# Kernel tuning notes

Hardware: AMD Instinct MI355X
Metric: run time of the kernel (lower is better)

The kernel has to match this reference:

```python
import jax, jax.numpy as jnp
import numpy as np

N_DIST, H, W, K = 256, 256, 192, 129
DR, DR0, DELTA = 0.2, 0.2, 1e-11


def _dual_exp(d, b1, b2, b3, b4):
    return b1 * np.exp(-b2 * d) + b3 * np.exp(-b4 * d)


def setup_inputs() -> dict:
    key = jax.random.key(0)
    d = (np.arange(N_DIST) + 1.0) * DR                      # distances (cm)
    gaus_amp = _dual_exp(d, 1.0, 0.01, 0.1, 0.001)
    gaus_sig = 0.05 * d + 1.0
    bkg_amp = _dual_exp(d, 0.05, 0.05, 0.01, 0.005)
    bkg_sig = 0.08 * d + 2.0
    xk = np.arange(-(K // 2), K // 2 + 1) * DR / DR0        # (K,) kernel coords
    # gaussian kernel (get_gaus_layer)
    kernel_g = np.sqrt(gaus_amp)[:, None] * np.exp(-xk[None, :] ** 2 / (2 * gaus_sig[:, None] ** 2 + DELTA))
    # background kernels (get_bkg_layers) with emulated splines
    w_f = lambda t: np.exp(-np.abs(t))
    iso_f = lambda t: 1.0 / (1.0 + t ** 2)
    xw = xk[None, :] / bkg_sig[:, None]
    kernel_w = bkg_amp[:, None] * (DR / DR0) * w_f(xw)
    kernel_iso = bkg_amp[:, None] * (DR / DR0) * iso_f(xw)
    # normalization factor (configure)
    xs = np.linspace(-5.0, 5.0, 2001)
    Iw = np.trapz(w_f(xs), xs)
    Iiso = np.trapz(iso_f(xs), xs)
    Nw = 3 * bkg_amp * Iw * bkg_sig
    Niso = bkg_amp * Iiso * bkg_sig
    Ng2 = gaus_amp * 2 * np.pi * gaus_sig ** 2 * (DR0 / DR) ** 2
    norm = (Nw + Niso ** 2 + 1.0) * Ng2
    x = jax.random.uniform(key, (1, N_DIST, H, W), dtype=jnp.float32)
    return {
        "x": x,
        "kernel_g": jnp.asarray(kernel_g, jnp.float32),
        "kernel_w": jnp.asarray(kernel_w, jnp.float32),
        "kernel_iso": jnp.asarray(kernel_iso, jnp.float32),
        "norm": jnp.asarray(norm, jnp.float32),
    }


def _dwconv(x, kern, axis):
    """Depthwise 'same' Conv1d along `axis` of (N,H,W); channels = dim 0."""
    n = x.shape[0]
    perm = (2, 0, 1) if axis == 1 else (1, 0, 2)   # -> (batch, channels=N, length)
    inv = (1, 2, 0) if axis == 1 else (1, 0, 2)
    xb = jnp.transpose(x, perm)
    y = jax.lax.conv_general_dilated(
        xb, kern[:, None, :], (1,), 'SAME',
        feature_group_count=n, dimension_numbers=('NCH', 'OIH', 'NCH'))
    return jnp.transpose(y, inv)


def _rotate(x, ang):
    """Bilinear rotation of (N,S,S) in dims (1,2), zero padding (grid_sample-like)."""
    s = x.shape[1]
    c = (s - 1) * 0.5
    ca, sa = jnp.cos(ang), jnp.sin(ang)
    idx = jnp.arange(s, dtype=x.dtype) - c
    yy, xx = jnp.meshgrid(idx, idx, indexing='ij')
    sy = ca * yy + sa * xx + c   # inverse-rotated source coords
    sx = -sa * yy + ca * xx + c
    y0 = jnp.floor(sy)
    x0 = jnp.floor(sx)
    fy, fx = sy - y0, sx - x0
    y0i, x0i = y0.astype(jnp.int32), x0.astype(jnp.int32)

    def gat(yi, xi):
        valid = (yi >= 0) & (yi < s) & (xi >= 0) & (xi < s)
        v = x[:, jnp.clip(yi, 0, s - 1), jnp.clip(xi, 0, s - 1)]
        return jnp.where(valid, v, 0.0)

    return (gat(y0i, x0i) * (1 - fy) * (1 - fx)
            + gat(y0i, x0i + 1) * (1 - fy) * fx
            + gat(y0i + 1, x0i) * fy * (1 - fx)
            + gat(y0i + 1, x0i + 1) * fy * fx)


def reference(x, kernel_g, kernel_w, kernel_iso, norm):
    out = x[0]                                   # (N, H, W)
    out = _dwconv(out, kernel_g, 1)
    out = _dwconv(out, kernel_g, 2)
    iso = _dwconv(out, kernel_iso, 1)
    iso = _dwconv(iso, kernel_iso, 2)
    n, h, w = out.shape
    pad = (n - w) // 2
    padded = jnp.pad(out, ((0, 0), (0, 0), (pad, pad)))  # (N, H, H) square plane
    tails = jnp.zeros_like(padded)
    for i in range(3):                            # 0, 60, 120 degrees
        ang = float(np.deg2rad(60 * i))
        t = _rotate(padded, ang)
        t = _dwconv(t, kernel_w, 2)
        tails = tails + _rotate(t, -ang)
    tails = tails[:, :, pad:pad + w]
    out = (out + tails + iso) / norm[:, None, None]
    return out[None]
```

## Files before the change

kernel.cpp:

```cpp
#include <hip/hip_runtime.h>
#include <cmath>

#define CN   256
#define HN   256
#define WN   192
#define KN   129
#define RN   64
#define SN   256
#define PADN 32

#define BBR 92
#define BBP 96


template <int TW, int WD, bool ACC>
__global__ __launch_bounds__(512, 2) void conv_w_blk(const float* __restrict__ in,
                                                     const float* __restrict__ kern,
                                                     float* __restrict__ out) {
    constexpr int NO    = TW / 8;
    constexpr int TOTB  = (NO + 128) / 8;
    constexpr int PITCH = 196;
    static_assert(NO == 16, "this instantiation is tuned for NO=16");
    __shared__ float lds[64 * PITCH + 132];
    float* __restrict__ ldsK = lds + 64 * PITCH;
    const int tid = threadIdx.x;
    const int x0  = blockIdx.x * TW;
    const int h0  = blockIdx.y * 64;
    const int c   = blockIdx.z;
    const float* __restrict__ in_c = in + ((size_t)c * HN + h0) * WD;

    if (tid < 132) ldsK[tid] = (tid < KN) ? kern[c * KN + tid] : 0.f;

    const int gc0 = max(0, x0 - 64);
    {
        const int srow = tid >> 3;
        const int scg  = tid & 7;
#pragma unroll
        for (int m = 0; m < 6; ++m) {
            const int c4 = scg + 8 * m;
            *(float4*)(lds + srow * PITCH + 4 * c4) =
                *(const float4*)(in_c + (size_t)srow * WD + gc0 + 4 * c4);
        }
    }
    __syncthreads();

    const int wv  = tid >> 6;
    const int l   = tid & 63;
    const int ac0 = x0 + wv * NO - 64;
    const int lbase = l * PITCH + (ac0 - gc0);

    float acc[NO];
#pragma unroll
    for (int t = 0; t < NO; ++t) acc[t] = 0.f;

    float X[8][8];

#define RD8(G)                                                                \
    if ((G) < TOTB) {                                                         \
        const int ac_ = ac0 + 8 * (G);                                        \
        if (ac_ >= 0 && ac_ + 8 <= WD) {             \
            const float4 a_ = *(const float4*)(lds + lbase + 8 * (G));        \
            const float4 b_ = *(const float4*)(lds + lbase + 8 * (G) + 4);    \
            X[(G) & 7][0] = a_.x; X[(G) & 7][1] = a_.y;                       \
            X[(G) & 7][2] = a_.z; X[(G) & 7][3] = a_.w;                       \
            X[(G) & 7][4] = b_.x; X[(G) & 7][5] = b_.y;                       \
            X[(G) & 7][6] = b_.z; X[(G) & 7][7] = b_.w;                       \
        } else {                                                              \
            _Pragma("unroll")                                                 \
            for (int i_ = 0; i_ < 8; ++i_) {                                  \
                const int cc_ = ac_ + i_;                                     \
                const int cl_ = min(max(cc_, 0), WD - 1);                     \
                const float v_ = lds[l * PITCH + (cl_ - gc0)];                \
                X[(G) & 7][i_] = (cc_ == cl_) ? v_ : 0.f;                     \
            }                                                                 \
        }                                                                     \
    }

    RD8(0) RD8(1) RD8(2) RD8(3) RD8(4) RD8(5)

    const float4* __restrict__ k4 = (const float4*)ldsK;
#pragma unroll
    for (int s = 0; s < 4; ++s) {
        float4 kc = k4[8 * s];
#pragma unroll
        for (int q = 0; q < 8; ++q) {
            float4 kn = (q < 7) ? k4[8 * s + q + 1] : kc;
#pragma unroll
            for (int u = 0; u < 4; ++u) {
                const float kj = (u == 0) ? kc.x : (u == 1) ? kc.y
                               : (u == 2) ? kc.z : kc.w;
#pragma unroll
                for (int t = 0; t < NO; ++t) {
                    const int e = 4 * q + u + t;
                    acc[t] = fmaf(X[(4 * s + e / 8) & 7][e % 8], kj, acc[t]);
                }
            }
            if (q == 0) { RD8(4 * s + 6) }
            if (q == 1) { RD8(4 * s + 7) }
            if (q == 2) { RD8(4 * s + 8) }
            if (q == 4) { RD8(4 * s + 9) }
            kc = kn;
        }
    }
    {
        const float k128 = ldsK[128];
#pragma unroll
        for (int t = 0; t < NO; ++t) {
            const int e = 32 + t;
            acc[t] = fmaf(X[(12 + e / 8) & 7][e % 8], k128, acc[t]);
        }
    }
#undef RD8

    __syncthreads();
#pragma unroll
    for (int i = 0; i < NO; i += 4)
        *(float4*)(lds + l * PITCH + wv * NO + i) =
            make_float4(acc[i], acc[i + 1], acc[i + 2], acc[i + 3]);
    __syncthreads();
    float* __restrict__ obase = out + ((size_t)c * HN + h0) * WD + x0;
    constexpr int NF4 = (64 * TW / 4) / 512;
#pragma unroll
    for (int k = 0; k < NF4; ++k) {
        const int i4  = k * 512 + tid;
        const int r   = i4 / (TW / 4);
        const int c4o = i4 - r * (TW / 4);
        float4 v = *(const float4*)(lds + r * PITCH + 4 * c4o);
        if (ACC) {
            const float4 o = *(const float4*)(obase + (size_t)r * WD + 4 * c4o);
            v.x += o.x; v.y += o.y; v.z += o.z; v.w += o.w;
        }
        *(float4*)(obase + (size_t)r * WD + 4 * c4o) = v;
    }
}

template <int TW, int WD, bool ACC>
__global__ __launch_bounds__(512, 2) void conv_w_lds(const float* __restrict__ in,
                                                     const float* __restrict__ kern,
                                                     float* __restrict__ out) {
    constexpr int NO    = TW / 8;
    constexpr int TWW   = TW + 128;
    constexpr int PITCH = TWW + 1;
    constexpr int NB    = (2 * NO + 31) / NO;
    __shared__ float lds[64 * PITCH + 132];
    float* __restrict__ ldsK = lds + 64 * PITCH;
    const int tid = threadIdx.x;
    const int x0  = blockIdx.x * TW;
    const int h0  = blockIdx.y * 64;
    const int c   = blockIdx.z;
    const float* __restrict__ in_c = in + ((size_t)c * HN + h0) * WD;

    if (tid < 132) ldsK[tid] = (tid < KN) ? kern[c * KN + tid] : 0.f;

    const int colg = tid & 63;
    const int rr   = tid >> 6;
    const int off  = x0 - 64;

    if (off >= 0 && off + TWW <= WD) {
#pragma unroll
        for (int m = 0; m < 4; ++m) {
            if (colg + 64 * m < TWW) {
#pragma unroll
                for (int k = 0; k < 8; ++k)
                    lds[(rr + 8 * k) * PITCH + colg + 64 * m] =
                        in_c[(size_t)(rr + 8 * k) * WD + off + colg + 64 * m];
            }
        }
    } else {
#pragma unroll
        for (int m = 0; m < 4; ++m) {
            if (colg + 64 * m < TWW) {
#pragma unroll
                for (int k = 0; k < 8; ++k) {
                    int g  = off + colg + 64 * m;
                    int gc = min(max(g, 0), WD - 1);
                    float v = in_c[(size_t)(rr + 8 * k) * WD + gc];
                    lds[(rr + 8 * k) * PITCH + colg + 64 * m] = (g == gc) ? v : 0.f;
                }
            }
        }
    }
    __syncthreads();

    const int wv = tid >> 6;
    const int l  = tid & 63;
    const int base = l * PITCH + wv * NO;

    float acc[NO];
#pragma unroll
    for (int t = 0; t < NO; ++t) acc[t] = 0.f;

    float H[4][NO];
    const float4* __restrict__ k4 = (const float4*)ldsK;
#pragma unroll
    for (int s = 0; s < 4; ++s) {
        const int sb = base + 32 * s;
#pragma unroll
        for (int k = 0; k < NB - 1; ++k)
#pragma unroll
            for (int i = 0; i < NO; ++i) H[k][i] = lds[sb + k * NO + i];
        float4 kc = k4[8 * s];
#pragma unroll
        for (int q = 0; q < 8; ++q) {
            float4 kn = (q < 7) ? k4[8 * s + q + 1] : kc;
#pragma unroll
            for (int u = 0; u < 4; ++u) {
                const int up = 4 * q + u;
                const float kj = (u == 0) ? kc.x : (u == 1) ? kc.y
                               : (u == 2) ? kc.z : kc.w;
#pragma unroll
                for (int t = 0; t < NO; ++t) {
                    const int e = up + t;
                    const float val = (e < NO)     ? H[0][e]
                                    : (e < 2 * NO) ? H[1][e - NO]
                                    : (e < 3 * NO) ? H[2][e - 2 * NO]
                                                   : H[3][e - 3 * NO];
                    acc[t] = fmaf(val, kj, acc[t]);
                }
            }
            if (q == 0) {
#pragma unroll
                for (int i = 0; i < NO; ++i)
                    H[NB - 1][i] = lds[sb + (NB - 1) * NO + i];
            }
            kc = kn;
        }
        if (s == 3) {
            const float k128 = ldsK[128];
#pragma unroll
            for (int t = 0; t < NO; ++t) {
                const int e = 32 + t;
                const float val = (e < NO)     ? H[0][e]
                                : (e < 2 * NO) ? H[1][e - NO]
                                : (e < 3 * NO) ? H[2][e - 2 * NO]
                                               : H[3][e - 3 * NO];
                acc[t] = fmaf(val, k128, acc[t]);
            }
        }
    }

    __syncthreads();
#pragma unroll
    for (int i = 0; i < NO; ++i) lds[base + i] = acc[i];
    __syncthreads();
    float* __restrict__ obase = out + ((size_t)c * HN + h0) * WD + x0;
#pragma unroll
    for (int k = 0; k < (64 * TW) / 512; ++k) {
        const int idx = k * 512 + tid;
        const int r  = idx / TW;
        const int cl = idx - r * TW;
        float v = lds[r * PITCH + cl];
        if (ACC) v += obase[(size_t)r * WD + cl];
        obase[(size_t)r * WD + cl] = v;
    }
}

__global__ __launch_bounds__(512, 2) void conv_h_lds(const float* __restrict__ in,
                                                     const float* __restrict__ kern,
                                                     float* __restrict__ out) {
    __shared__ float lds[256 * 64 + 132];
    float* __restrict__ ldsK = lds + 256 * 64;
    const int tid = threadIdx.x;
    const int x0  = blockIdx.x * 64;
    const int h0  = blockIdx.y * 128;
    const int c   = blockIdx.z;
    const float* __restrict__ in_c = in + (size_t)c * HN * WN + x0;

    if (tid < 132) ldsK[tid] = (tid < KN) ? kern[c * KN + tid] : 0.f;

    {
        const int f4 = (tid & 15) * 4;
        const int rw = tid >> 4;
        const int off = h0 - 64;
#pragma unroll
        for (int p = 0; p < 8; ++p) {
            const int lr = rw + 32 * p;
            const int g  = off + lr;
            const int gc = min(max(g, 0), HN - 1);
            float4 v = *(const float4*)(in_c + (size_t)gc * WN + f4);
            if (g != gc) { v.x = 0.f; v.y = 0.f; v.z = 0.f; v.w = 0.f; }
            *(float4*)(lds + lr * 64 + f4) = v;
        }
    }
    __syncthreads();

    const int W = (tid >> 6) * 16;
    const int l = tid & 63;

    float acc[16];
#pragma unroll
    for (int t = 0; t < 16; ++t) acc[t] = 0.f;

    float X0[16], X1[16], X2[16], X3[16];

#define RD16(BUF, b)                                                          \
    { _Pragma("unroll")                                                       \
      for (int i = 0; i < 16; ++i) BUF[i] = lds[(W + 16 * (b) + i) * 64 + l]; }

#define STG(s, LOW, MID, HIGH, NXT, hasNxt)                                   \
    {                                                                         \
        const float4* __restrict__ k4 = (const float4*)ldsK;                  \
        float4 kc = k4[8 * (s)];                                              \
        _Pragma("unroll")                                                     \
        for (int q = 0; q < 8; ++q) {                                         \
            float4 kn = (q < 7) ? k4[8 * (s) + q + 1] : kc;                   \
            _Pragma("unroll")                                                 \
            for (int u = 0; u < 4; ++u) {                                     \
                const float kj = (u == 0) ? kc.x : (u == 1) ? kc.y            \
                               : (u == 2) ? kc.z : kc.w;                      \
                _Pragma("unroll")                                             \
                for (int t = 0; t < 16; ++t) {                                \
                    const int e = 4 * q + u + t;                              \
                    const float val = (e < 16) ? LOW[e]                       \
                                    : (e < 32) ? MID[e - 16] : HIGH[e - 32];  \
                    acc[t] = fmaf(val, kj, acc[t]);                           \
                }                                                             \
            }                                                                 \
            if (q == 0) RD16(HIGH, 2 * (s) + 2)                               \
            if ((hasNxt) && q == 1) RD16(NXT, 2 * (s) + 3)                    \
            kc = kn;                                                          \
        }                                                                     \
    }

    RD16(X0, 0)
    RD16(X1, 1)
    STG(0, X0, X1, X2, X3, true)
    STG(1, X2, X3, X0, X1, true)
    STG(2, X0, X1, X2, X3, true)
    STG(3, X2, X3, X0, X1, false)
#undef RD16
#undef STG

    {
        const float k128 = ldsK[128];
#pragma unroll
        for (int t = 0; t < 16; ++t) acc[t] = fmaf(X0[t], k128, acc[t]);
    }

    float* __restrict__ ob = out + ((size_t)c * HN + h0 + W) * WN + x0 + l;
#pragma unroll
    for (int t = 0; t < 16; ++t) ob[(size_t)t * WN] = acc[t];
}

__global__ __launch_bounds__(256) void rot_fwd_lds(const float* __restrict__ Cin,
                                                   float* __restrict__ out,
                                                   float ca, float sa) {
    __shared__ float tile[BBR * BBP];
    const int j0 = blockIdx.x * 64;
    const int i0 = blockIdx.y * 64;
    const int c  = blockIdx.z;
    const float cc = (SN - 1) * 0.5f;
    const float yA = (float)i0 - cc, yB = (float)(i0 + 63) - cc;
    const float xA = (float)j0 - cc, xB = (float)(j0 + 63) - cc;
    const float syAA = ca * yA + sa * xA + cc, syAB = ca * yA + sa * xB + cc;
    const float syBA = ca * yB + sa * xA + cc, syBB = ca * yB + sa * xB + cc;
    const float sxAA = -sa * yA + ca * xA + cc, sxAB = -sa * yA + ca * xB + cc;
    const float sxBA = -sa * yB + ca * xA + cc, sxBB = -sa * yB + ca * xB + cc;
    const int ybase = (int)floorf(fminf(fminf(syAA, syAB), fminf(syBA, syBB))) - 1;
    const int xbase = (int)floorf(fminf(fminf(sxAA, sxAB), fminf(sxBA, sxBB))) - 1;

    const float* __restrict__ base = Cin + (size_t)c * HN * WN;
    for (int t = threadIdx.x; t < BBR * BBP; t += 256) {
        const int r  = t / BBP;
        const int q  = t - r * BBP;
        const int gy = ybase + r;
        const int gx = xbase + q - PADN;
        float v = 0.f;
        if ((unsigned)gy < (unsigned)HN && (unsigned)gx < (unsigned)WN)
            v = base[(size_t)gy * WN + gx];
        tile[t] = v;
    }
    __syncthreads();

    const int l  = threadIdx.x & 63;
    const int r0 = threadIdx.x >> 6;
    const int j  = j0 + l;
    const float xx = (float)j - cc;
    float* __restrict__ ocol = out + (size_t)c * SN * SN + j;
#pragma unroll
    for (int t = 0; t < 16; ++t) {
        const int i = i0 + r0 + 4 * t;
        const float yy = (float)i - cc;
        const float sy = ca * yy + sa * xx + cc;
        const float sx = -sa * yy + ca * xx + cc;
        const float y0f = floorf(sy), x0f = floorf(sx);
        const float fy = sy - y0f, fx = sx - x0f;
        const int ly = (int)y0f - ybase;
        const int lx = (int)x0f - xbase;
        const float* p = tile + ly * BBP + lx;
        const float v00 = p[0], v01 = p[1], v10 = p[BBP], v11 = p[BBP + 1];
        ocol[(size_t)i * SN] = (1.f - fy) * ((1.f - fx) * v00 + fx * v01)
                             + fy * ((1.f - fx) * v10 + fx * v11);
    }
}

template <bool FINAL>
__global__ __launch_bounds__(256) void rot_bwd_lds(const float* __restrict__ U,
                                                   float* __restrict__ dst,
                                                   const float* __restrict__ accIn,
                                                   const float* __restrict__ norm,
                                                   float ca, float sa) {
    __shared__ float tile[BBR * BBP];
    const int x0 = blockIdx.x * 64;
    const int i0 = blockIdx.y * 64;
    const int c  = blockIdx.z;
    const float cc = (SN - 1) * 0.5f;
    const float yA = (float)i0 - cc, yB = (float)(i0 + 63) - cc;
    const float xA = (float)(x0 + PADN) - cc, xB = (float)(x0 + PADN + 63) - cc;
    const float syAA = ca * yA + sa * xA + cc, syAB = ca * yA + sa * xB + cc;
    const float syBA = ca * yB + sa * xA + cc, syBB = ca * yB + sa * xB + cc;
    const float sxAA = -sa * yA + ca * xA + cc, sxAB = -sa * yA + ca * xB + cc;
    const float sxBA = -sa * yB + ca * xA + cc, sxBB = -sa * yB + ca * xB + cc;
    const int ybase = (int)floorf(fminf(fminf(syAA, syAB), fminf(syBA, syBB))) - 1;
    const int xbase = (int)floorf(fminf(fminf(sxAA, sxAB), fminf(sxBA, sxBB))) - 1;

    const float* __restrict__ base = U + (size_t)c * SN * SN;
    for (int t = threadIdx.x; t < BBR * BBP; t += 256) {
        const int r  = t / BBP;
        const int q  = t - r * BBP;
        const int gy = ybase + r;
        const int gx = xbase + q;
        float v = 0.f;
        if ((unsigned)gy < (unsigned)SN && (unsigned)gx < (unsigned)SN)
            v = base[(size_t)gy * SN + gx];
        tile[t] = v;
    }
    __syncthreads();

    const int l  = threadIdx.x & 63;
    const int r0 = threadIdx.x >> 6;
    const int xc = x0 + l;
    const float xx = (float)(xc + PADN) - cc;
    float inv = 0.f;
    if constexpr (FINAL) inv = 1.f / norm[c];
#pragma unroll
    for (int t = 0; t < 16; ++t) {
        const int i = i0 + r0 + 4 * t;
        const float yy = (float)i - cc;
        const float sy = ca * yy + sa * xx + cc;
        const float sx = -sa * yy + ca * xx + cc;
        const float y0f = floorf(sy), x0f = floorf(sx);
        const float fy = sy - y0f, fx = sx - x0f;
        const int ly = (int)y0f - ybase;
        const int lx = (int)x0f - xbase;
        const float* p = tile + ly * BBP + lx;
        const float v00 = p[0], v01 = p[1], v10 = p[BBP], v11 = p[BBP + 1];
        const float val = (1.f - fy) * ((1.f - fx) * v00 + fx * v01)
                        + fy * ((1.f - fx) * v10 + fx * v11);
        const size_t idx = ((size_t)c * HN + i) * WN + xc;
        if constexpr (FINAL) {
            dst[idx] = (dst[idx] + accIn[idx] + val) * inv;
        } else {
            dst[idx] += val;
        }
    }
}

extern "C" void kernel_launch(void* const* d_in, const int* in_sizes, int n_in,
                              void* d_out, int out_size, void* d_ws, size_t ws_size,
                              hipStream_t stream) {
    const float* x    = (const float*)d_in[0];
    const float* kg   = (const float*)d_in[1];
    const float* kw   = (const float*)d_in[2];
    const float* kiso = (const float*)d_in[3];
    const float* norm = (const float*)d_in[4];

    float* C = (float*)d_out;
    float* ws = (float*)d_ws;
    const size_t IMG = (size_t)CN * HN * WN;
    const size_t PSQ = (size_t)CN * SN * SN;
    float* B   = ws;
    float* acc = ws + IMG;
    float* T   = ws + 2 * IMG;
    float* U   = T + PSQ;

    const dim3 blk256(256);
    const dim3 blk512(512);
    const dim3 convHGrid(WN / 64, HN / 128, CN);
    const dim3 convW192Grid(2, HN / 64, CN);
    const dim3 convW256Grid(2, HN / 64, CN);
    const dim3 rotFGrid(SN / 64, SN / 64, CN);
    const dim3 rotBGrid(WN / 64, HN / 64, CN);

    conv_h_lds<<<convHGrid, blk512, 0, stream>>>(x, kg, B);
    conv_w_lds<96, WN, false><<<convW192Grid, blk512, 0, stream>>>(B, kg, C);
    conv_h_lds<<<convHGrid, blk512, 0, stream>>>(C, kiso, B);
    conv_w_lds<96, WN, false><<<convW192Grid, blk512, 0, stream>>>(B, kiso, acc);
    conv_w_lds<96, WN, true><<<convW192Grid, blk512, 0, stream>>>(C, kw, acc);
    const double a1 = 60.0 * M_PI / 180.0, a2 = 120.0 * M_PI / 180.0;
    const float c1 = (float)cos(a1), s1 = (float)sin(a1);
    const float c2 = (float)cos(a2), s2 = (float)sin(a2);

    rot_fwd_lds<<<rotFGrid, blk256, 0, stream>>>(C, T, c1, s1);
    conv_w_blk<128, SN, false><<<convW256Grid, blk512, 0, stream>>>(T, kw, U);
    rot_bwd_lds<false><<<rotBGrid, blk256, 0, stream>>>(U, acc, nullptr, nullptr, c1, -s1);

    rot_fwd_lds<<<rotFGrid, blk256, 0, stream>>>(C, T, c2, s2);
    conv_w_blk<128, SN, false><<<convW256Grid, blk512, 0, stream>>>(T, kw, U);
    rot_bwd_lds<true><<<rotBGrid, blk256, 0, stream>>>(U, C, acc, norm, c2, -s2);

    (void)in_sizes; (void)n_in; (void)out_size; (void)ws_size;
}
```

Before: 690.7 us.

## Process full column height per block in H convolution with 32-row register tiles

The H-direction convolution now handles all 256 rows of a 64-column strip in one block instead of splitting the height into two 128-row halves. This removes the duplicated halo loads, since each half previously loaded 256 rows for 128 outputs. Each thread now computes 32 outputs from two 32-element register buffers, with zero-padding moved from the global load into the LDS read. This doubles accumulator and buffer registers, which risks lower occupancy or spills. It also halves the block count and drops the interleaved prefetch of the next rows.

```diff
diff --git a/kernel.cpp b/kernel.cpp
--- a/kernel.cpp
+++ b/kernel.cpp
@@ -262,8 +262,7 @@
     float* __restrict__ ldsK = lds + 256 * 64;
     const int tid = threadIdx.x;
     const int x0  = blockIdx.x * 64;
-    const int h0  = blockIdx.y * 128;
-    const int c   = blockIdx.z;
+    const int c   = blockIdx.y;
     const float* __restrict__ in_c = in + (size_t)c * HN * WN + x0;
 
     if (tid < 132) ldsK[tid] = (tid < KN) ? kern[c * KN + tid] : 0.f;
@@ -271,33 +270,43 @@
     {
         const int f4 = (tid & 15) * 4;
         const int rw = tid >> 4;
-        const int off = h0 - 64;
 #pragma unroll
         for (int p = 0; p < 8; ++p) {
-            const int lr = rw + 32 * p;
-            const int g  = off + lr;
-            const int gc = min(max(g, 0), HN - 1);
-            float4 v = *(const float4*)(in_c + (size_t)gc * WN + f4);
-            if (g != gc) { v.x = 0.f; v.y = 0.f; v.z = 0.f; v.w = 0.f; }
-            *(float4*)(lds + lr * 64 + f4) = v;
-        }
-    }
-    __syncthreads();
-
-    const int W = (tid >> 6) * 16;
-    const int l = tid & 63;
-
-    float acc[16];
-#pragma unroll
-    for (int t = 0; t < 16; ++t) acc[t] = 0.f;
-
-    float X0[16], X1[16], X2[16], X3[16];
-
-#define RD16(BUF, b)                                                          \
-    { _Pragma("unroll")                                                       \
-      for (int i = 0; i < 16; ++i) BUF[i] = lds[(W + 16 * (b) + i) * 64 + l]; }
-
-#define STG(s, LOW, MID, HIGH, NXT, hasNxt)                                   \
+            const int r = rw + 32 * p;
+            *(float4*)(lds + r * 64 + f4) =
+                *(const float4*)(in_c + (size_t)r * WN + f4);
+        }
+    }
+    __syncthreads();
+
+    const int wv = tid >> 6;
+    const int l  = tid & 63;
+    const int rbase = wv * 32 - 64;
+
+    float acc[32];
+#pragma unroll
+    for (int t = 0; t < 32; ++t) acc[t] = 0.f;
+
+    float B0[32], B1[32];
+
+#define RDBLK(BUF, rfirst)                                                    \
+    {                                                                         \
+        const int rf = (rfirst);                                              \
+        if (rf >= 0 && rf + 31 < HN) {                                        \
+            _Pragma("unroll")                                                 \
+            for (int i = 0; i < 32; ++i) BUF[i] = lds[(rf + i) * 64 + l];     \
+        } else {                                                              \
+            _Pragma("unroll")                                                 \
+            for (int i = 0; i < 32; ++i) {                                    \
+                const int r  = rf + i;                                        \
+                const int rc = min(max(r, 0), HN - 1);                        \
+                const float v = lds[rc * 64 + l];                             \
+                BUF[i] = (r == rc) ? v : 0.f;                                 \
+            }                                                                 \
+        }                                                                     \
+    }
+
+#define STAGE(s, LOW, HIGH)                                                   \
     {                                                                         \
         const float4* __restrict__ k4 = (const float4*)ldsK;                  \
         float4 kc = k4[8 * (s)];                                              \
@@ -309,37 +318,36 @@
                 const float kj = (u == 0) ? kc.x : (u == 1) ? kc.y            \
                                : (u == 2) ? kc.z : kc.w;                      \
                 _Pragma("unroll")                                             \
-                for (int t = 0; t < 16; ++t) {                                \
+                for (int t = 0; t < 32; ++t) {                                \
                     const int e = 4 * q + u + t;                              \
-                    const float val = (e < 16) ? LOW[e]                       \
-                                    : (e < 32) ? MID[e - 16] : HIGH[e - 32];  \
+                    const float val = (e < 32) ? LOW[e] : HIGH[e - 32];       \
                     acc[t] = fmaf(val, kj, acc[t]);                           \
                 }                                                             \
             }                                                                 \
-            if (q == 0) RD16(HIGH, 2 * (s) + 2)                               \
-            if ((hasNxt) && q == 1) RD16(NXT, 2 * (s) + 3)                    \
             kc = kn;                                                          \
         }                                                                     \
     }
 
-    RD16(X0, 0)
-    RD16(X1, 1)
-    STG(0, X0, X1, X2, X3, true)
-    STG(1, X2, X3, X0, X1, true)
-    STG(2, X0, X1, X2, X3, true)
-    STG(3, X2, X3, X0, X1, false)
-#undef RD16
-#undef STG
-
+    RDBLK(B0, rbase);
+    RDBLK(B1, rbase + 32);
+    STAGE(0, B0, B1);
+    RDBLK(B0, rbase + 64);
+    STAGE(1, B1, B0);
+    RDBLK(B1, rbase + 96);
+    STAGE(2, B0, B1);
+    RDBLK(B0, rbase + 128);
+    STAGE(3, B1, B0);
     {
         const float k128 = ldsK[128];
 #pragma unroll
-        for (int t = 0; t < 16; ++t) acc[t] = fmaf(X0[t], k128, acc[t]);
-    }
-
-    float* __restrict__ ob = out + ((size_t)c * HN + h0 + W) * WN + x0 + l;
-#pragma unroll
-    for (int t = 0; t < 16; ++t) ob[(size_t)t * WN] = acc[t];
+        for (int t = 0; t < 32; ++t) acc[t] = fmaf(B0[t], k128, acc[t]);
+    }
+#undef RDBLK
+#undef STAGE
+
+    float* __restrict__ ob = out + ((size_t)c * HN + wv * 32) * WN + x0 + l;
+#pragma unroll
+    for (int t = 0; t < 32; ++t) ob[(size_t)t * WN] = acc[t];
 }
 
 __global__ __launch_bounds__(256) void rot_fwd_lds(const float* __restrict__ Cin,
@@ -476,7 +484,7 @@
 
     const dim3 blk256(256);
     const dim3 blk512(512);
-    const dim3 convHGrid(WN / 64, HN / 128, CN);
+    const dim3 convHGrid(WN / 64, CN);
     const dim3 convW192Grid(2, HN / 64, CN);
     const dim3 convW256Grid(2, HN / 64, CN);
     const dim3 rotFGrid(SN / 64, SN / 64, CN);
```

New measurement: 732.4 us. +6.0%, slower.
